# Optimization experiments

Hardware: AMD Instinct MI355X
Metric: run time of the kernel (lower is better)

## Reference

```python
import jax, jax.numpy as jnp
import numpy as np

EPS = 1e-5

def _layernorm(x, w, b):
    mu = jnp.mean(x, axis=-1, keepdims=True)
    var = jnp.mean(jnp.square(x - mu), axis=-1, keepdims=True)
    return (x - mu) * jax.lax.rsqrt(var + EPS) * w + b

def setup_inputs() -> dict:
    key = jax.random.key(0)
    ks = jax.random.split(key, 6)
    B, Np, Nc, D, P = 2, 512, 512, 128, 128
    p_embed = jax.random.normal(ks[0], (B, Np, D), dtype=jnp.float32)
    c_embed = jax.random.normal(ks[1], (B, Nc, D), dtype=jnp.float32)
    p_mask = jnp.ones((B, Np), dtype=bool)
    c_mask = jnp.ones((B, Nc), dtype=bool)
    ln_p_w = jnp.ones((D,), jnp.float32)
    ln_p_b = jnp.zeros((D,), jnp.float32)
    ln_c_w = jnp.ones((D,), jnp.float32)
    ln_c_b = jnp.zeros((D,), jnp.float32)
    W_out = jax.random.normal(ks[2], (P, D), dtype=jnp.float32) / np.sqrt(D)
    b_out = jax.random.normal(ks[3], (P,), dtype=jnp.float32) * 0.01
    return {"p_embed": p_embed, "c_embed": c_embed, "p_mask": p_mask,
            "c_mask": c_mask, "ln_p_w": ln_p_w, "ln_p_b": ln_p_b,
            "ln_c_w": ln_c_w, "ln_c_b": ln_c_b, "W_out": W_out, "b_out": b_out}

def reference(p_embed, c_embed, p_mask, c_mask, ln_p_w, ln_p_b, ln_c_w, ln_c_b, W_out, b_out):
    # inter_mask[b,i,j] = p_mask[b,i] & c_mask[b,j]
    inter_mask = p_mask[..., :, None] & c_mask[..., None, :]
    p = _layernorm(p_embed, ln_p_w, ln_p_b)  # [B,Np,D]
    c = _layernorm(c_embed, ln_c_w, ln_c_b)  # [B,Nc,D]
    # einsum '...ik,...jk->...ijk' followed by Linear(D->P), fused into one
    # contraction so the [B,Np,Nc,D] intermediate is never materialized:
    # out[b,i,j,h] = sum_k p[b,i,k]*c[b,j,k]*W_out[h,k] + b_out[h]
    inter = jnp.einsum('bik,bjk,hk->bijh', p, c, W_out) + b_out
    inter = inter * inter_mask[..., None].astype(inter.dtype)
    return inter, inter_mask
```

## Files before the change

kernel.cpp:

```cpp
#include <hip/hip_runtime.h>
#include <hip/hip_bf16.h>

#define BATCH 2
#define NP 512
#define NC 512
#define DD 128
#define PP 128

typedef __bf16 bf16_t;
typedef __bf16 bf16x8 __attribute__((ext_vector_type(8)));
typedef __bf16 bf16x2 __attribute__((ext_vector_type(2)));
typedef float f32x4 __attribute__((ext_vector_type(4)));

__global__ __launch_bounds__(64) void ln_kernel(
    const float* __restrict__ p, const float* __restrict__ c,
    const float* __restrict__ pw, const float* __restrict__ pb,
    const float* __restrict__ cw, const float* __restrict__ cb,
    float* __restrict__ p_ln, bf16_t* __restrict__ c_bf) {
    int row = blockIdx.x;
    bool isP = row < BATCH * NP;
    int crow = row - BATCH * NP;
    const float* x  = isP ? p + (size_t)row * DD : c + (size_t)crow * DD;
    const float* w  = isP ? pw : cw;
    const float* bs = isP ? pb : cb;
    int t = threadIdx.x;
    float2 v = *(const float2*)&x[2 * t];
    float s  = v.x + v.y;
    float sq = v.x * v.x + v.y * v.y;
    for (int o = 32; o; o >>= 1) {
        s  += __shfl_xor(s, o);
        sq += __shfl_xor(sq, o);
    }
    float mu  = s * (1.0f / 128.0f);
    float var = sq * (1.0f / 128.0f) - mu * mu;
    float rs  = rsqrtf(var + 1e-5f);
    float2 wv = *(const float2*)&w[2 * t];
    float2 bv = *(const float2*)&bs[2 * t];
    float o0 = (v.x - mu) * rs * wv.x + bv.x;
    float o1 = (v.y - mu) * rs * wv.y + bv.y;
    if (isP) {
        float2 o2; o2.x = o0; o2.y = o1;
        *(float2*)&p_ln[(size_t)row * DD + 2 * t] = o2;
    } else {
        bf16x2 o2; o2[0] = (bf16_t)o0; o2[1] = (bf16_t)o1;
        *(bf16x2*)&c_bf[(size_t)crow * DD + 2 * t] = o2;
    }
}

__global__ __launch_bounds__(256, 4) void inter_kernel(
    const float* __restrict__ p_ln, const bf16_t* __restrict__ c_bf,
    const float* __restrict__ W, const float* __restrict__ b_out,
    const int* __restrict__ p_mask,
    const int* __restrict__ c_mask,
    float* __restrict__ out) {
    int blk = blockIdx.x;
    int i = blk & (NP - 1);
    int b = blk >> 9;
    int t = threadIdx.x;
    int lane = t & 63;
    int wave = t >> 6;
    int l16 = lane & 15, q = lane >> 4;

    int pm = p_mask[b * NP + i];

    const float* pr = p_ln + ((size_t)(b * NP + i)) * DD;
    bf16x8 wf[2][4];
    #pragma unroll
    for (int ht = 0; ht < 2; ++ht) {
        int h = wave * 32 + ht * 16 + l16;
        const float* wr = W + (size_t)h * DD;
        #pragma unroll
        for (int kt = 0; kt < 4; ++kt) {
            int k = kt * 32 + q * 8;
            float4 w0 = *(const float4*)&wr[k];
            float4 w1 = *(const float4*)&wr[k + 4];
            float4 pv0 = *(const float4*)&pr[k];
            float4 pv1 = *(const float4*)&pr[k + 4];
            bf16x8 f;
            f[0] = (bf16_t)(w0.x * pv0.x); f[1] = (bf16_t)(w0.y * pv0.y);
            f[2] = (bf16_t)(w0.z * pv0.z); f[3] = (bf16_t)(w0.w * pv0.w);
            f[4] = (bf16_t)(w1.x * pv1.x); f[5] = (bf16_t)(w1.y * pv1.y);
            f[6] = (bf16_t)(w1.z * pv1.z); f[7] = (bf16_t)(w1.w * pv1.w);
            wf[ht][kt] = f;
        }
    }

    f32x4 bias0 = *(const f32x4*)&b_out[wave * 32 + q * 4];
    f32x4 bias1 = *(const f32x4*)&b_out[wave * 32 + 16 + q * 4];

    const bf16_t* cbb = c_bf + (size_t)b * NC * DD;
    const int* cmb = c_mask + b * NC;
    size_t outbase = (((size_t)b * NP + i) * NC) * PP;

    #pragma unroll 2
    for (int jt = 0; jt < NC / 16; ++jt) {
        int j = jt * 16 + l16;
        bf16x8 cf[4];
        #pragma unroll
        for (int kt = 0; kt < 4; ++kt)
            cf[kt] = *(const bf16x8*)&cbb[(size_t)j * DD + kt * 32 + q * 8];
        f32x4 acc0 = {0.f, 0.f, 0.f, 0.f};
        f32x4 acc1 = {0.f, 0.f, 0.f, 0.f};
        #pragma unroll
        for (int kt = 0; kt < 4; ++kt) {
            acc0 = __builtin_amdgcn_mfma_f32_16x16x32_bf16(wf[0][kt], cf[kt], acc0, 0, 0, 0);
            acc1 = __builtin_amdgcn_mfma_f32_16x16x32_bf16(wf[1][kt], cf[kt], acc1, 0, 0, 0);
        }
        float scale = (pm != 0 && cmb[j] != 0) ? 1.0f : 0.0f;
        float* orow = out + outbase + (size_t)j * PP + wave * 32 + q * 4;
        *(f32x4*)&orow[0]  = (acc0 + bias0) * scale;
        *(f32x4*)&orow[16] = (acc1 + bias1) * scale;
    }

    size_t mbase = (size_t)BATCH * NP * NC * PP;
    for (int jj = t; jj < NC; jj += 256) {
        out[mbase + ((size_t)b * NP + i) * NC + jj] =
            (pm != 0 && cmb[jj] != 0) ? 1.0f : 0.0f;
    }
}

extern "C" void kernel_launch(void* const* d_in, const int* in_sizes, int n_in,
                              void* d_out, int out_size, void* d_ws, size_t ws_size,
                              hipStream_t stream) {
    const float* p_embed = (const float*)d_in[0];
    const float* c_embed = (const float*)d_in[1];
    const int* p_mask = (const int*)d_in[2];
    const int* c_mask = (const int*)d_in[3];
    const float* ln_p_w = (const float*)d_in[4];
    const float* ln_p_b = (const float*)d_in[5];
    const float* ln_c_w = (const float*)d_in[6];
    const float* ln_c_b = (const float*)d_in[7];
    const float* W_out  = (const float*)d_in[8];
    const float* b_out  = (const float*)d_in[9];
    float* out = (float*)d_out;

    float* p_ln = (float*)d_ws;
    bf16_t* c_bf = (bf16_t*)(p_ln + (size_t)BATCH * NP * DD);

    ln_kernel<<<BATCH * (NP + NC), 64, 0, stream>>>(
        p_embed, c_embed, ln_p_w, ln_p_b, ln_c_w, ln_c_b, p_ln, c_bf);
    inter_kernel<<<BATCH * NP, 256, 0, stream>>>(
        p_ln, c_bf, W_out, b_out, p_mask, c_mask, out);
}
```

Before: 316.9 us.

## Split j dimension across blocks and stage c tile in LDS

Each block now handles one (b,i) row and a 128-wide chunk of j instead of all 512 j, giving four times as many blocks. The block's 128x128 bf16 c tile is cooperatively loaded into padded shared memory, and MFMA operands are read from LDS instead of global memory. Masks are precomputed into registers. This raises parallelism and cuts redundant global reads of c. In exchange, each block repeats the W*p fragment setup and pays a barrier plus about 34KB of LDS, which may limit occupancy.

```diff
diff --git a/kernel.cpp b/kernel.cpp
--- a/kernel.cpp
+++ b/kernel.cpp
@@ -53,15 +53,36 @@
     const int* __restrict__ p_mask,
     const int* __restrict__ c_mask,
     float* __restrict__ out) {
+    __shared__ bf16_t As[128][136];
+
     int blk = blockIdx.x;
-    int i = blk & (NP - 1);
-    int b = blk >> 9;
+    int jq = blk & 3;
+    int i  = (blk >> 2) & (NP - 1);
+    int b  = blk >> 11;
+    int j0 = jq * 128;
+
     int t = threadIdx.x;
     int lane = t & 63;
     int wave = t >> 6;
     int l16 = lane & 15, q = lane >> 4;
 
+    const bf16_t* cbb = c_bf + ((size_t)(b * NC + j0)) * DD;
+    {
+        int col = (t & 15) * 8;
+        int rg = t >> 4;
+        #pragma unroll
+        for (int pass = 0; pass < 8; ++pass) {
+            int r = pass * 16 + rg;
+            *(bf16x8*)&As[r][col] = *(const bf16x8*)&cbb[(size_t)r * DD + col];
+        }
+    }
+
     int pm = p_mask[b * NP + i];
+    const int* cmb = c_mask + b * NC + j0;
+    float sc[8];
+    #pragma unroll
+    for (int jt = 0; jt < 8; ++jt)
+        sc[jt] = (pm != 0 && cmb[jt * 16 + l16] != 0) ? 1.0f : 0.0f;
 
     const float* pr = p_ln + ((size_t)(b * NP + i)) * DD;
     bf16x8 wf[2][4];
@@ -88,17 +109,16 @@
     f32x4 bias0 = *(const f32x4*)&b_out[wave * 32 + q * 4];
     f32x4 bias1 = *(const f32x4*)&b_out[wave * 32 + 16 + q * 4];
 
-    const bf16_t* cbb = c_bf + (size_t)b * NC * DD;
-    const int* cmb = c_mask + b * NC;
-    size_t outbase = (((size_t)b * NP + i) * NC) * PP;
+    __syncthreads();
 
+    size_t outbase = (((size_t)b * NP + i) * NC + j0) * PP;
     #pragma unroll 2
-    for (int jt = 0; jt < NC / 16; ++jt) {
-        int j = jt * 16 + l16;
+    for (int jt = 0; jt < 8; ++jt) {
+        int jr = jt * 16 + l16;
         bf16x8 cf[4];
         #pragma unroll
         for (int kt = 0; kt < 4; ++kt)
-            cf[kt] = *(const bf16x8*)&cbb[(size_t)j * DD + kt * 32 + q * 8];
+            cf[kt] = *(const bf16x8*)&As[jr][kt * 32 + q * 8];
         f32x4 acc0 = {0.f, 0.f, 0.f, 0.f};
         f32x4 acc1 = {0.f, 0.f, 0.f, 0.f};
         #pragma unroll
@@ -106,16 +126,15 @@
             acc0 = __builtin_amdgcn_mfma_f32_16x16x32_bf16(wf[0][kt], cf[kt], acc0, 0, 0, 0);
             acc1 = __builtin_amdgcn_mfma_f32_16x16x32_bf16(wf[1][kt], cf[kt], acc1, 0, 0, 0);
         }
-        float scale = (pm != 0 && cmb[j] != 0) ? 1.0f : 0.0f;
-        float* orow = out + outbase + (size_t)j * PP + wave * 32 + q * 4;
-        *(f32x4*)&orow[0]  = (acc0 + bias0) * scale;
-        *(f32x4*)&orow[16] = (acc1 + bias1) * scale;
+        float* orow = out + outbase + (size_t)jr * PP + wave * 32 + q * 4;
+        *(f32x4*)&orow[0]  = (acc0 + bias0) * sc[jt];
+        *(f32x4*)&orow[16] = (acc1 + bias1) * sc[jt];
     }
 
-    size_t mbase = (size_t)BATCH * NP * NC * PP;
-    for (int jj = t; jj < NC; jj += 256) {
-        out[mbase + ((size_t)b * NP + i) * NC + jj] =
-            (pm != 0 && cmb[jj] != 0) ? 1.0f : 0.0f;
+    if (t < 128) {
+        size_t mbase = (size_t)BATCH * NP * NC * PP;
+        out[mbase + ((size_t)b * NP + i) * NC + j0 + t] =
+            (pm != 0 && cmb[t] != 0) ? 1.0f : 0.0f;
     }
 }
 
@@ -139,6 +158,6 @@
 
     ln_kernel<<<BATCH * (NP + NC), 64, 0, stream>>>(
         p_embed, c_embed, ln_p_w, ln_p_b, ln_c_w, ln_c_b, p_ln, c_bf);
-    inter_kernel<<<BATCH * NP, 256, 0, stream>>>(
+    inter_kernel<<<BATCH * NP * (NC / 128), 256, 0, stream>>>(
         p_ln, c_bf, W_out, b_out, p_mask, c_mask, out);
 }
```

Measured after the change: 302.1 us. 1.05x faster.
